# Kernel optimization log

Measured on AMD Instinct MI355X. Metric: run time of the kernel, lower is better.

## Reference

```python
import jax, jax.numpy as jnp
import numpy as np

RES = 32          # resolution (32, 32) -> N = 1024 tokens
HEADS = 16
EMB = 1024
BATCH = 8
N = RES * RES


def _bias_idxs(res):
    # relative-offset index table, [N, N] with values in [0, res*res)
    coords = np.stack(np.meshgrid(np.arange(res), np.arange(res), indexing='ij'), -1).reshape(-1, 2)
    d = np.abs(coords[:, None, :] - coords[None, :, :])  # [N, N, 2]
    return jnp.asarray(d[..., 0] * res + d[..., 1], dtype=jnp.int64)


def setup_inputs() -> dict:
    key = jax.random.key(0)
    k1, k2, k3, k4, k5 = jax.random.split(key, 5)
    x = jax.random.normal(k1, (BATCH, N, EMB), dtype=jnp.float32)
    w_qkv = jax.random.normal(k2, (3 * EMB, EMB), dtype=jnp.float32) * 0.02
    biases = jax.random.normal(k3, (HEADS, RES * RES), dtype=jnp.float32) * 0.02
    bias_idxs = _bias_idxs(RES)
    w_out = jax.random.normal(k4, (EMB, EMB), dtype=jnp.float32) * 0.02
    b_out = jax.random.normal(k5, (EMB,), dtype=jnp.float32) * 0.02
    return {"x": x, "w_qkv": w_qkv, "biases": biases,
            "bias_idxs": bias_idxs, "w_out": w_out, "b_out": b_out}


def reference(x, w_qkv, biases, bias_idxs, w_out, b_out):
    b, n, e = x.shape
    h = HEADS
    d = e // h
    scale = d ** -0.5
    # to_qkv: Linear(e, 3e, bias=False); torch Linear computes x @ W.T
    qkv = x @ w_qkv.T                                   # [b, n, 3e]
    q, k, v = jnp.split(qkv, 3, axis=-1)
    def to_heads(t):
        return t.reshape(b, n, h, d).transpose(0, 2, 1, 3)  # b h n d
    q, k, v = to_heads(q), to_heads(k), to_heads(v)
    scores = jnp.einsum('bhid,bhjd->bhij', q, k) * scale    # [b, h, n, n]
    scores = scores + biases[:, bias_idxs]                  # gather -> [h, n, n], broadcast over b
    attn = jax.nn.softmax(scores, axis=-1)
    out = jnp.einsum('bhij,bhjd->bhid', attn, v)            # [b, h, n, d]
    out = out.transpose(0, 2, 1, 3).reshape(b, n, e)        # b n (h d)
    # to_out: Linear(e, e) with bias (dropout = identity at inference)
    return out @ w_out.T + b_out
```

## Files before the change

### kernel.cpp

```cpp
#include <hip/hip_runtime.h>
#include <stdint.h>


#define LOG2E 1.4426950408889634f

typedef __attribute__((ext_vector_type(8))) short short8;
typedef __attribute__((ext_vector_type(4))) short short4v;
typedef __attribute__((ext_vector_type(4))) float floatx4;

__device__ __forceinline__ short f2bf(float f) {
  uint32_t u = __builtin_bit_cast(uint32_t, f);
  u = (u + 0x7FFFu + ((u >> 16) & 1u)) >> 16;
  return (short)(uint16_t)u;
}
__device__ __forceinline__ float bf2f(short s) {
  uint32_t u = ((uint32_t)(uint16_t)s) << 16;
  return __builtin_bit_cast(float, u);
}

__device__ __forceinline__ void gload_lds16(const short* g, short* l) {
  __builtin_amdgcn_global_load_lds(
      (const __attribute__((address_space(1))) void*)g,
      (__attribute__((address_space(3))) void*)l, 16, 0, 0);
}

__global__ void cvt_bf16(const float* __restrict__ src, short* __restrict__ dst, int n4) {
  int i = blockIdx.x * 256 + threadIdx.x;
  if (i >= n4) return;
  float4 f = ((const float4*)src)[i];
  short4v o;
  o.x = f2bf(f.x); o.y = f2bf(f.y); o.z = f2bf(f.z); o.w = f2bf(f.w);
  ((short4v*)dst)[i] = o;
}

__global__ void bias_precomp(const float* __restrict__ biases, short* __restrict__ biast) {
  int t = blockIdx.x * 256 + threadIdx.x;
  int lane = t & 63;
  int tile = t >> 6;
  int jt = tile & 63, it = (tile >> 6) & 63, h = tile >> 12;
  int i0 = it * 16 + ((lane >> 4) << 2);
  int j = jt * 16 + (lane & 15);
  int rj = j >> 5, cj = j & 31;
  short4v o;
#pragma unroll
  for (int r = 0; r < 4; r++) {
    int i = i0 + r;
    int ri = i >> 5, ci = i & 31;
    int dr = ri - rj; if (dr < 0) dr = -dr;
    int dc = ci - cj; if (dc < 0) dc = -dc;
    o[r] = f2bf(biases[h * 1024 + dr * 32 + dc] * LOG2E);
  }
  *(short4v*)&biast[(size_t)t * 4] = o;
}

template <int MODE>
__global__ __launch_bounds__(256, 2) void gemm_bt(
    const short* __restrict__ A, const short* __restrict__ Bt,
    short* __restrict__ qo, short* __restrict__ ko, short* __restrict__ vto,
    const float* __restrict__ bvec, float* __restrict__ outf) {
  __shared__ __align__(16) short sA[128 * 64];
  __shared__ __align__(16) short sB[128 * 64];
  const int tid = threadIdx.x;
  const int w = tid >> 6, lane = tid & 63;
  const int wr = w >> 1, wc = w & 1;
  const int bm = blockIdx.y, bn = blockIdx.x;
  const int qd = lane >> 4, col = lane & 15;

  floatx4 acc[4][4] = {};
  const int rowA0 = bm * 128, rowB0 = bn * 128;
  const int ciw = w * 256;

  for (int kk = 0; kk < 1024; kk += 64) {
    __syncthreads();
#pragma unroll
    for (int n = 0; n < 4; n++) {
      int ci = ciw + n * 64 + lane;
      int r = ci >> 3, c = (ci & 7) ^ (r & 7);
      gload_lds16(A + (size_t)(rowA0 + r) * 1024 + kk + c * 8, &sA[ci * 8]);
    }
#pragma unroll
    for (int n = 0; n < 4; n++) {
      int ci = ciw + n * 64 + lane;
      int r = ci >> 3, c = (ci & 7) ^ (r & 7);
      gload_lds16(Bt + (size_t)(rowB0 + r) * 1024 + kk + c * 8, &sB[ci * 8]);
    }
    __syncthreads();

#pragma unroll
    for (int ks = 0; ks < 2; ks++) {
      const int ch = qd + ks * 4;
      short8 af[4], bff[4];
#pragma unroll
      for (int rt = 0; rt < 4; rt++) {
        int r = wr * 64 + rt * 16 + col;
        af[rt] = *(const short8*)&sA[r * 64 + ((ch ^ (r & 7)) << 3)];
      }
#pragma unroll
      for (int ct = 0; ct < 4; ct++) {
        int r = wc * 64 + ct * 16 + col;
        bff[ct] = *(const short8*)&sB[r * 64 + ((ch ^ (r & 7)) << 3)];
      }
#pragma unroll
      for (int rt = 0; rt < 4; rt++)
#pragma unroll
        for (int ct = 0; ct < 4; ct++)
          acc[rt][ct] = __builtin_amdgcn_mfma_f32_16x16x32_bf16(af[rt], bff[ct], acc[rt][ct], 0, 0, 0);
    }
  }

  if (MODE == 0) {
    if (bn >= 16) {
#pragma unroll
      for (int rt = 0; rt < 4; rt++) {
#pragma unroll
        for (int ct = 0; ct < 4; ct++) {
          int Cg = bn * 128 + wc * 64 + ct * 16 + col;
          int e = Cg & 1023, h = e >> 6, dd = e & 63;
          short4v pv;
#pragma unroll
          for (int r = 0; r < 4; r++) pv[r] = f2bf(acc[rt][ct][r]);
          int R0 = bm * 128 + wr * 64 + rt * 16 + qd * 4;
          int b = R0 >> 10, n0 = R0 & 1023;
          int bh = b * 16 + h;
          *(short4v*)&vto[((size_t)bh * 64 + dd) * 1024 + n0] = pv;
        }
      }
    } else {
#pragma unroll
      for (int rt = 0; rt < 4; rt++) {
#pragma unroll
        for (int ct = 0; ct < 4; ct++) {
          int Cg = bn * 128 + wc * 64 + ct * 16 + col;
          int which = Cg >> 10, e = Cg & 1023, h = e >> 6, dd = e & 63;
#pragma unroll
          for (int r = 0; r < 4; r++) {
            int R = bm * 128 + wr * 64 + rt * 16 + qd * 4 + r;
            int b = R >> 10, n = R & 1023;
            int bh = b * 16 + h;
            short v = f2bf(acc[rt][ct][r]);
            if (which == 0)
              qo[((size_t)bh * 1024 + n) * 64 + dd] = v;
            else
              ko[((size_t)bh * 1024 + n) * 64 + dd] = v;
          }
        }
      }
    }
  } else {
#pragma unroll
    for (int rt = 0; rt < 4; rt++)
#pragma unroll
      for (int ct = 0; ct < 4; ct++) {
        int Cg = bn * 128 + wc * 64 + ct * 16 + col;
        float bo = bvec[Cg];
#pragma unroll
        for (int r = 0; r < 4; r++) {
          int R = bm * 128 + wr * 64 + rt * 16 + qd * 4 + r;
          outf[(size_t)R * 1024 + Cg] = acc[rt][ct][r] + bo;
        }
      }
  }
}

__global__ __launch_bounds__(256, 2) void attn_fused(
    const short* __restrict__ q, const short* __restrict__ k,
    const short* __restrict__ vt, const short* __restrict__ biast,
    short* __restrict__ ao) {
  __shared__ __align__(16) short sQ[128 * 64];
  __shared__ __align__(16) short sK[128 * 64];
  __shared__ __align__(16) short sVt[64 * 128];
  __shared__ __align__(16) short sP[128 * 128];
  const int tid = threadIdx.x, w = tid >> 6, lane = tid & 63;
  const int bh = blockIdx.x, qt = blockIdx.y;
  const int h = bh & 15;
  const int qd = lane >> 4, col = lane & 15;
  const short* qb = q + (size_t)bh * 65536;
  const short* kb = k + (size_t)bh * 65536;
  const short* vb = vt + (size_t)bh * 65536;
  const int ciw = w * 256;

#pragma unroll
  for (int n = 0; n < 4; n++) {
    int ci = ciw + n * 64 + lane;
    int r = ci >> 3, c = (ci & 7) ^ (r & 7);
    gload_lds16(qb + (size_t)(qt * 128 + r) * 64 + c * 8, &sQ[ci * 8]);
  }

  floatx4 oacc[2][4] = {};
  float lsum[8] = {0, 0, 0, 0, 0, 0, 0, 0};
  const float SCL = 0.125f * LOG2E;

  for (int js = 0; js < 8; js++) {
    __syncthreads();
#pragma unroll
    for (int n = 0; n < 4; n++) {
      int ci = ciw + n * 64 + lane;
      int r = ci >> 3, c = (ci & 7) ^ (r & 7);
      gload_lds16(kb + (size_t)(js * 128 + r) * 64 + c * 8, &sK[ci * 8]);
    }
#pragma unroll
    for (int n = 0; n < 4; n++) {
      int ci = ciw + n * 64 + lane;
      int r = ci >> 4, c = (ci & 15) ^ (r & 15);
      gload_lds16(vb + (size_t)r * 1024 + js * 128 + c * 8, &sVt[ci * 8]);
    }
    __syncthreads();

    short4v bfrag[2][8];
#pragma unroll
    for (int rt = 0; rt < 2; rt++) {
      int a = js * 8 + w * 2 + rt;
#pragma unroll
      for (int ct = 0; ct < 8; ct++) {
        int b = qt * 8 + ct;
        bfrag[rt][ct] = *(const short4v*)&biast[((((size_t)h * 64 + a) * 64 + b) << 8) + lane * 4];
      }
    }

    floatx4 sacc[2][8] = {};
#pragma unroll
    for (int ks = 0; ks < 2; ks++) {
      const int ch = qd + ks * 4;
      short8 ak[2], bq[8];
#pragma unroll
      for (int rt = 0; rt < 2; rt++) {
        int r = w * 32 + rt * 16 + col;
        ak[rt] = *(const short8*)&sK[r * 64 + ((ch ^ (r & 7)) << 3)];
      }
#pragma unroll
      for (int ct = 0; ct < 8; ct++) {
        int r2 = ct * 16 + col;
        bq[ct] = *(const short8*)&sQ[r2 * 64 + ((ch ^ (r2 & 7)) << 3)];
      }
#pragma unroll
      for (int rt = 0; rt < 2; rt++)
#pragma unroll
        for (int ct = 0; ct < 8; ct++)
          sacc[rt][ct] = __builtin_amdgcn_mfma_f32_16x16x32_bf16(ak[rt], bq[ct], sacc[rt][ct], 0, 0, 0);
    }

#pragma unroll
    for (int rt = 0; rt < 2; rt++) {
      int s = w * 8 + rt * 4 + qd;
#pragma unroll
      for (int ct = 0; ct < 8; ct++) {
        int i = ct * 16 + col;
        short4v pb;
#pragma unroll
        for (int r = 0; r < 4; r++) {
          float e = exp2f(fmaf(sacc[rt][ct][r], SCL, bf2f(bfrag[rt][ct][r])));
          lsum[ct] += e;
          pb[r] = f2bf(e);
        }
        *(short4v*)&sP[i * 128 + ((s ^ ((i & 7) << 1)) << 2)] = pb;
      }
    }
    __syncthreads();

#pragma unroll
    for (int ks = 0; ks < 4; ks++) {
      const int ch = ks * 4 + qd;
      short8 ap[2], bv[4];
#pragma unroll
      for (int rt = 0; rt < 2; rt++) {
        int m = w * 32 + rt * 16 + col;
        ap[rt] = *(const short8*)&sP[m * 128 + ((ch ^ (m & 7)) << 3)];
      }
#pragma unroll
      for (int ct = 0; ct < 4; ct++) {
        int d = ct * 16 + col;
        bv[ct] = *(const short8*)&sVt[d * 128 + ((ch ^ (d & 15)) << 3)];
      }
#pragma unroll
      for (int rt = 0; rt < 2; rt++)
#pragma unroll
        for (int ct = 0; ct < 4; ct++)
          oacc[rt][ct] = __builtin_amdgcn_mfma_f32_16x16x32_bf16(ap[rt], bv[ct], oacc[rt][ct], 0, 0, 0);
    }
  }

#pragma unroll
  for (int ct = 0; ct < 8; ct++) {
    float v = lsum[ct];
    v += __shfl_xor(v, 16);
    v += __shfl_xor(v, 32);
    lsum[ct] = v;
  }
  float* red = (float*)sQ;
  if (lane < 16) {
#pragma unroll
    for (int ct = 0; ct < 8; ct++) red[w * 128 + ct * 16 + lane] = lsum[ct];
  }
  __syncthreads();

  float inv[2][4];
#pragma unroll
  for (int rt = 0; rt < 2; rt++)
#pragma unroll
    for (int r = 0; r < 4; r++) {
      int i = w * 32 + rt * 16 + qd * 4 + r;
      float t = red[i] + red[128 + i] + red[256 + i] + red[384 + i];
      inv[rt][r] = 1.0f / t;
    }

  const int b = bh >> 4;
#pragma unroll
  for (int rt = 0; rt < 2; rt++)
#pragma unroll
    for (int ct = 0; ct < 4; ct++)
#pragma unroll
      for (int r = 0; r < 4; r++) {
        int n = qt * 128 + w * 32 + rt * 16 + qd * 4 + r;
        int dd = ct * 16 + col;
        ao[(((size_t)b * 1024 + n) << 10) + h * 64 + dd] = f2bf(oacc[rt][ct][r] * inv[rt][r]);
      }
}

extern "C" void kernel_launch(void* const* d_in, const int* in_sizes, int n_in,
                              void* d_out, int out_size, void* d_ws, size_t ws_size,
                              hipStream_t stream) {
  const float* x = (const float*)d_in[0];
  const float* w_qkv = (const float*)d_in[1];
  const float* biases = (const float*)d_in[2];
  const float* w_out = (const float*)d_in[4];
  const float* b_out = (const float*)d_in[5];
  float* out = (float*)d_out;

  char* ws = (char*)d_ws;
  short* xb    = (short*)(ws + 0);
  short* wqkvb = (short*)(ws + 16777216);
  short* woutb = (short*)(ws + 23068672);
  short* qb    = (short*)(ws + 25165824);
  short* kb    = (short*)(ws + 41943040);
  short* vtb   = (short*)(ws + 58720256);
  short* aob   = (short*)(ws + 75497472);
  short* biast = (short*)(ws + 92274688);

  cvt_bf16<<<8192, 256, 0, stream>>>(x, xb, 8192 * 1024 / 4);
  cvt_bf16<<<3072, 256, 0, stream>>>(w_qkv, wqkvb, 3072 * 1024 / 4);
  cvt_bf16<<<1024, 256, 0, stream>>>(w_out, woutb, 1024 * 1024 / 4);
  bias_precomp<<<16384, 256, 0, stream>>>(biases, biast);

  gemm_bt<0><<<dim3(24, 64), 256, 0, stream>>>(xb, wqkvb, qb, kb, vtb, nullptr, nullptr);
  attn_fused<<<dim3(128, 8), 256, 0, stream>>>(qb, kb, vtb, biast, aob);
  gemm_bt<1><<<dim3(8, 64), 256, 0, stream>>>(aob, woutb, nullptr, nullptr, nullptr, b_out, out);
}
```

Baseline: 269.2 us.

## Keep Q fragments in registers, pad P tile, use fast exp2 and packed bf16 stores

Loads the Q tile once into registers (bq) for the whole key loop instead of rereading it from LDS every iteration, and reuses the P buffer to stage Q so the separate sQ array is dropped. The P tile switches from an XOR swizzle to row padding (stride 136), and the score loop is reorganised per row tile to shorten the lifetime of the accumulators. Exp uses the hardware exp2 builtin, and the bf16 conversion becomes round-half-up with perm packing. This cuts LDS traffic and ALU work but adds 64 VGPRs of Q fragments, which risks lower occupancy under launch_bounds(256,2), and it changes bf16 rounding slightly.

```diff
diff --git a/kernel.cpp b/kernel.cpp
--- a/kernel.cpp
+++ b/kernel.cpp
@@ -7,6 +7,7 @@
 typedef __attribute__((ext_vector_type(8))) short short8;
 typedef __attribute__((ext_vector_type(4))) short short4v;
 typedef __attribute__((ext_vector_type(4))) float floatx4;
+typedef __attribute__((ext_vector_type(2))) unsigned int uint2v;
 
 __device__ __forceinline__ short f2bf(float f) {
   uint32_t u = __builtin_bit_cast(uint32_t, f);
@@ -16,6 +17,13 @@
 __device__ __forceinline__ float bf2f(short s) {
   uint32_t u = ((uint32_t)(uint16_t)s) << 16;
   return __builtin_bit_cast(float, u);
+}
+__device__ __forceinline__ float fast_exp2(float x) {
+#if __has_builtin(__builtin_amdgcn_exp2f)
+  return __builtin_amdgcn_exp2f(x);
+#else
+  return exp2f(x);
+#endif
 }
 
 __device__ __forceinline__ void gload_lds16(const short* g, short* l) {
@@ -166,10 +174,9 @@
     const short* __restrict__ q, const short* __restrict__ k,
     const short* __restrict__ vt, const short* __restrict__ biast,
     short* __restrict__ ao) {
-  __shared__ __align__(16) short sQ[128 * 64];
   __shared__ __align__(16) short sK[128 * 64];
   __shared__ __align__(16) short sVt[64 * 128];
-  __shared__ __align__(16) short sP[128 * 128];
+  __shared__ __align__(16) short sP[128 * 136];
   const int tid = threadIdx.x, w = tid >> 6, lane = tid & 63;
   const int bh = blockIdx.x, qt = blockIdx.y;
   const int h = bh & 15;
@@ -183,7 +190,18 @@
   for (int n = 0; n < 4; n++) {
     int ci = ciw + n * 64 + lane;
     int r = ci >> 3, c = (ci & 7) ^ (r & 7);
-    gload_lds16(qb + (size_t)(qt * 128 + r) * 64 + c * 8, &sQ[ci * 8]);
+    gload_lds16(qb + (size_t)(qt * 128 + r) * 64 + c * 8, &sP[ci * 8]);
+  }
+  __syncthreads();
+  short8 bq[2][8];
+#pragma unroll
+  for (int ks = 0; ks < 2; ks++) {
+    const int ch = qd + ks * 4;
+#pragma unroll
+    for (int ct = 0; ct < 8; ct++) {
+      int r2 = ct * 16 + col;
+      bq[ks][ct] = *(const short8*)&sP[r2 * 64 + ((ch ^ (r2 & 7)) << 3)];
+    }
   }
 
   floatx4 oacc[2][4] = {};
@@ -217,42 +235,35 @@
       }
     }
 
-    floatx4 sacc[2][8] = {};
-#pragma unroll
-    for (int ks = 0; ks < 2; ks++) {
-      const int ch = qd + ks * 4;
-      short8 ak[2], bq[8];
-#pragma unroll
-      for (int rt = 0; rt < 2; rt++) {
+#pragma unroll
+    for (int rt = 0; rt < 2; rt++) {
+      floatx4 sacc[8] = {};
+#pragma unroll
+      for (int ks = 0; ks < 2; ks++) {
+        const int ch = qd + ks * 4;
         int r = w * 32 + rt * 16 + col;
-        ak[rt] = *(const short8*)&sK[r * 64 + ((ch ^ (r & 7)) << 3)];
-      }
-#pragma unroll
-      for (int ct = 0; ct < 8; ct++) {
-        int r2 = ct * 16 + col;
-        bq[ct] = *(const short8*)&sQ[r2 * 64 + ((ch ^ (r2 & 7)) << 3)];
-      }
-#pragma unroll
-      for (int rt = 0; rt < 2; rt++)
+        short8 ak = *(const short8*)&sK[r * 64 + ((ch ^ (r & 7)) << 3)];
 #pragma unroll
         for (int ct = 0; ct < 8; ct++)
-          sacc[rt][ct] = __builtin_amdgcn_mfma_f32_16x16x32_bf16(ak[rt], bq[ct], sacc[rt][ct], 0, 0, 0);
-    }
-
-#pragma unroll
-    for (int rt = 0; rt < 2; rt++) {
-      int s = w * 8 + rt * 4 + qd;
+          sacc[ct] = __builtin_amdgcn_mfma_f32_16x16x32_bf16(ak, bq[ks][ct], sacc[ct], 0, 0, 0);
+      }
+      const int s = w * 8 + rt * 4 + qd;
 #pragma unroll
       for (int ct = 0; ct < 8; ct++) {
         int i = ct * 16 + col;
-        short4v pb;
-#pragma unroll
-        for (int r = 0; r < 4; r++) {
-          float e = exp2f(fmaf(sacc[rt][ct][r], SCL, bf2f(bfrag[rt][ct][r])));
-          lsum[ct] += e;
-          pb[r] = f2bf(e);
-        }
-        *(short4v*)&sP[i * 128 + ((s ^ ((i & 7) << 1)) << 2)] = pb;
+        float e0 = fast_exp2(fmaf(sacc[ct][0], SCL, bf2f(bfrag[rt][ct][0])));
+        float e1 = fast_exp2(fmaf(sacc[ct][1], SCL, bf2f(bfrag[rt][ct][1])));
+        float e2 = fast_exp2(fmaf(sacc[ct][2], SCL, bf2f(bfrag[rt][ct][2])));
+        float e3 = fast_exp2(fmaf(sacc[ct][3], SCL, bf2f(bfrag[rt][ct][3])));
+        lsum[ct] += (e0 + e1) + (e2 + e3);
+        uint32_t u0 = __builtin_bit_cast(uint32_t, e0) + 0x8000u;
+        uint32_t u1 = __builtin_bit_cast(uint32_t, e1) + 0x8000u;
+        uint32_t u2 = __builtin_bit_cast(uint32_t, e2) + 0x8000u;
+        uint32_t u3 = __builtin_bit_cast(uint32_t, e3) + 0x8000u;
+        uint2v pk;
+        pk.x = __builtin_amdgcn_perm(u1, u0, 0x07060302u);
+        pk.y = __builtin_amdgcn_perm(u3, u2, 0x07060302u);
+        *(uint2v*)&sP[i * 136 + s * 4] = pk;
       }
     }
     __syncthreads();
@@ -264,7 +275,7 @@
 #pragma unroll
       for (int rt = 0; rt < 2; rt++) {
         int m = w * 32 + rt * 16 + col;
-        ap[rt] = *(const short8*)&sP[m * 128 + ((ch ^ (m & 7)) << 3)];
+        ap[rt] = *(const short8*)&sP[m * 136 + ch * 8];
       }
 #pragma unroll
       for (int ct = 0; ct < 4; ct++) {
@@ -286,7 +297,7 @@
     v += __shfl_xor(v, 32);
     lsum[ct] = v;
   }
-  float* red = (float*)sQ;
+  float* red = (float*)sK;
   if (lane < 16) {
 #pragma unroll
     for (int ct = 0; ct < 8; ct++) red[w * 128 + ct * 16 + lane] = lsum[ct];
@@ -299,7 +310,7 @@
 #pragma unroll
     for (int r = 0; r < 4; r++) {
       int i = w * 32 + rt * 16 + qd * 4 + r;
-      float t = red[i] + red[128 + i] + red[256 + i] + red[384 + i];
+      float t = (red[i] + red[128 + i]) + (red[256 + i] + red[384 + i]);
       inv[rt][r] = 1.0f / t;
     }
 
```

New measurement: 272.0 us. About the same (+1.0%).
